# Performance work log

Measured on AMD Instinct MI355X. Metric: run time of the kernel, lower is better.

## Reference

```python
import jax, jax.numpy as jnp
import numpy as np

N_NODES = 50000
N_EDGES = 300000
D = 256          # in_dim = out_dim (residual)
DE = 256         # edge relation dim
K = 2            # num_kgs
H = 4            # heads
L = 2            # layers
DH = D // H


def _routed_linear(x, W, b, idx):
    # x:[E,din], W:[K,din,dout], b:[K,dout], idx:[E] in [0,K)
    # Compute all K branches (K is tiny) then select per edge.
    outs = jnp.einsum('ed,kdo->keo', x, W) + b[:, None, :]
    return outs[idx, jnp.arange(idx.shape[0])]


def _layernorm(x, g, b):
    mu = jnp.mean(x, axis=-1, keepdims=True)
    var = jnp.mean(jnp.square(x - mu), axis=-1, keepdims=True)
    return (x - mu) * jax.lax.rsqrt(var + 1e-5) * g + b


def _mga_layer(h, src, dst, kg_src, kg_dst, beta, rel,
               ln_g, ln_b, Wt, bt, Wq, bq, Wk, bk):
    N = h.shape[0]
    E = src.shape[0]
    residual = h
    hn = _layernorm(h, ln_g, ln_b)
    x_j = hn[src]                       # [E,D] gathered source feats
    x_i = hn[dst]                       # [E,D] gathered target feats
    # per-edge KG-routed transfer of concatenated (x_j, relation emb)
    xj_t = jax.nn.gelu(_routed_linear(jnp.concatenate([x_j, rel], axis=1), Wt, bt, kg_src),
                       approximate=False)
    q = _routed_linear(x_i, Wq, bq, kg_dst).reshape(E, H, DH)
    k = _routed_linear(xj_t, Wk, bk, kg_src).reshape(E, H, DH)
    # per-edge multi-head dot product, scaled by edge_beta_r then 1/sqrt(dh)
    att = jnp.sum(q * k, axis=-1) * beta[:, None] / jnp.sqrt(jnp.asarray(DH, h.dtype))  # [E,H]
    # scatter-softmax over incoming edges of each target node
    m = jax.ops.segment_max(att, dst, num_segments=N)          # [N,H]
    e = jnp.exp(att - m[dst])
    denom = jax.ops.segment_sum(e, dst, num_segments=N)        # [N,H]
    a = e / (denom[dst] + 1e-16)                                # [E,H]
    msg = (a[:, :, None] * xj_t.reshape(E, H, DH)).reshape(E, D)
    aggr = jax.ops.segment_sum(msg, dst, num_segments=N)        # [N,D]
    return residual + jax.nn.gelu(aggr, approximate=False)


def setup_inputs() -> dict:
    key = jax.random.key(0)
    ks = jax.random.split(key, 10)
    x = jax.random.normal(ks[0], (N_NODES, D), dtype=jnp.float32)
    edge_index = jax.random.randint(ks[1], (2, N_EDGES), 0, N_NODES, dtype=jnp.int32)
    edge_kg_index = jax.random.randint(ks[2], (2, N_EDGES), 0, K, dtype=jnp.int32)
    edge_beta_r = jax.random.uniform(ks[3], (N_EDGES,), dtype=jnp.float32)
    edge_rel_emb = jax.random.normal(ks[4], (N_EDGES, DE), dtype=jnp.float32)
    return {
        'x': x,
        'edge_index': edge_index,
        'edge_kg_index': edge_kg_index,
        'edge_beta_r': edge_beta_r,
        'edge_rel_emb': edge_rel_emb,
        'ln_g': jnp.ones((L, D), jnp.float32),
        'ln_b': jnp.zeros((L, D), jnp.float32),
        'Wt': jax.random.normal(ks[5], (L, K, D + DE, D), jnp.float32) / np.sqrt(D + DE),
        'bt': jnp.zeros((L, K, D), jnp.float32),
        'Wq': jax.random.normal(ks[6], (L, K, D, D), jnp.float32) / np.sqrt(D),
        'bq': jnp.zeros((L, K, D), jnp.float32),
        'Wk': jax.random.normal(ks[7], (L, K, D, D), jnp.float32) / np.sqrt(D),
        'bk': jnp.zeros((L, K, D), jnp.float32),
    }


def reference(x, edge_index, edge_kg_index, edge_beta_r, edge_rel_emb,
              ln_g, ln_b, Wt, bt, Wq, bq, Wk, bk):
    src, dst = edge_index[0], edge_index[1]          # j (source), i (target)
    kg_src, kg_dst = edge_kg_index[0], edge_kg_index[1]
    h = x  # dropout is identity in eval mode
    for l in range(L):
        h = _mga_layer(h, src, dst, kg_src, kg_dst, edge_beta_r, edge_rel_emb,
                       ln_g[l], ln_b[l], Wt[l], bt[l], Wq[l], bq[l], Wk[l], bk[l])
    return h
```

## Files before the change

kernel.cpp:

```cpp
#include <hip/hip_runtime.h>
#include <hip/hip_bf16.h>

#define NN 50000
#define NE 300000
#define DD 256
#define NCHUNK 293

typedef __hip_bfloat16 bf16;
typedef __attribute__((ext_vector_type(8))) short bf16x8;
typedef __attribute__((ext_vector_type(4))) float f32x4;

__device__ __forceinline__ float bf2f(bf16 v) { return __bfloat162float(v); }
__device__ __forceinline__ unsigned short f2b(float v) {
    bf16 t = __float2bfloat16(v);
    return *reinterpret_cast<unsigned short*>(&t);
}
__device__ __forceinline__ float b2f_bits(unsigned short u) {
    return __uint_as_float(((unsigned)u) << 16);
}
__device__ __forceinline__ float gelu_f(float v) {
    float v2 = v * v;
    float z  = v * fmaf(v2, 0.044715f, 1.0f) * 0.7978845608f;
    float e  = __expf(2.0f * z);
    float th = 1.0f - 2.0f / (e + 1.0f);
    return 0.5f * v * (1.0f + th);
}
__device__ __forceinline__ void gl2lds16(const uint4* g, uint4* l) {
    __builtin_amdgcn_global_load_lds(
        (const __attribute__((address_space(1))) void*)g,
        (__attribute__((address_space(3))) void*)l, 16, 0, 0);
}

__global__ void part_count(const int* __restrict__ kg, int* __restrict__ bcnt) {
    int base = blockIdx.x * 1024;
    __shared__ int wc[4];
    int t = threadIdx.x, wave = t >> 6, lane = t & 63;
    int cnt = 0;
    #pragma unroll
    for (int s = 0; s < 4; ++s) {
        int j = base + s * 256 + t;
        int is0 = (j < NE && kg[j] == 0) ? 1 : 0;
        unsigned long long m = __ballot(is0);
        if (lane == 0) cnt += __popcll(m);
    }
    if (lane == 0) wc[wave] = cnt;
    __syncthreads();
    if (t == 0) bcnt[blockIdx.x] = wc[0] + wc[1] + wc[2] + wc[3];
}

__global__ __launch_bounds__(512) void part_scan(const int* __restrict__ bcnt,
                                                 int* __restrict__ bofs,
                                                 int* __restrict__ meta, int n) {
    __shared__ int tmp[512];
    int t = threadIdx.x;
    int v = (t < n) ? bcnt[t] : 0;
    tmp[t] = v;
    __syncthreads();
    #pragma unroll
    for (int off = 1; off < 512; off <<= 1) {
        int u = (t >= off) ? tmp[t - off] : 0;
        __syncthreads();
        tmp[t] += u;
        __syncthreads();
    }
    if (t < n) bofs[t] = tmp[t] - v;
    if (t == n - 1) meta[0] = tmp[t];
}

__global__ void part_scatter(const int* __restrict__ kg, const int* __restrict__ bofs,
                             const int* __restrict__ meta, int* __restrict__ perm) {
    int base = blockIdx.x * 1024;
    int c0 = meta[0];
    __shared__ int wz[4];
    int t = threadIdx.x, wave = t >> 6, lane = t & 63;
    int zrun = bofs[blockIdx.x];
    for (int s = 0; s < 4; ++s) {
        int j = base + s * 256 + t;
        int valid = j < NE;
        int is0 = (valid && kg[j] == 0) ? 1 : 0;
        unsigned long long m = __ballot(is0);
        int zb = __popcll(m & ((1ull << lane) - 1ull));
        if (lane == 0) wz[wave] = __popcll(m);
        __syncthreads();
        int wbefore = 0;
        for (int w = 0; w < wave; ++w) wbefore += wz[w];
        int zeros_before = zrun + wbefore + zb;
        if (valid) {
            int pos = is0 ? zeros_before : (c0 + (j - zeros_before));
            perm[pos] = j;
        }
        int stepz = wz[0] + wz[1] + wz[2] + wz[3];
        __syncthreads();
        zrun += stepz;
    }
}

__global__ void deg_hist(const int* __restrict__ dst, int* __restrict__ deg) {
    int i = blockIdx.x * blockDim.x + threadIdx.x;
    if (i < NE) atomicAdd(&deg[dst[i]], 1);
}

__global__ __launch_bounds__(1024) void scan_nodes(const int* __restrict__ deg,
                                                   int* __restrict__ ofs,
                                                   int* __restrict__ cur) {
    __shared__ int pex[1025];
    int t = threadIdx.x;
    const int C = (NN + 1023) / 1024;
    int base = t * C;
    int s = 0;
    for (int j = 0; j < C; ++j) { int idx = base + j; if (idx < NN) s += deg[idx]; }
    pex[t + 1] = s;
    __syncthreads();
    if (t == 0) {
        pex[0] = 0;
        for (int i = 1; i <= 1024; ++i) pex[i] += pex[i - 1];
    }
    __syncthreads();
    int run = pex[t];
    for (int j = 0; j < C; ++j) {
        int idx = base + j;
        if (idx < NN) { ofs[idx] = run; cur[idx] = run; run += deg[idx]; }
    }
    if (t == 1023) ofs[NN] = pex[1024];
}

__global__ void csr_fill(const int* __restrict__ dst, int* __restrict__ cur,
                         int* __restrict__ eid) {
    int i = blockIdx.x * blockDim.x + threadIdx.x;
    if (i < NE) {
        int p = atomicAdd(&cur[dst[i]], 1);
        eid[p] = i;
    }
}

__global__ void f2b_vec_kernel(const float* __restrict__ in, ushort* __restrict__ out, long n4) {
    long i0 = (long)blockIdx.x * blockDim.x + threadIdx.x;
    long stride = (long)gridDim.x * blockDim.x;
    for (long i = i0; i < n4; i += stride) {
        float4 v = ((const float4*)in)[i];
        ushort4 o;
        o.x = f2b(v.x); o.y = f2b(v.y); o.z = f2b(v.z); o.w = f2b(v.w);
        ((ushort4*)out)[i] = o;
    }
}

__global__ void transpose_w_kernel(const float* __restrict__ in, ushort* __restrict__ out,
                                   int shift, long total) {
    long i0 = (long)blockIdx.x * blockDim.x + threadIdx.x;
    long stride = (long)gridDim.x * blockDim.x;
    long dmask = ((long)1 << shift) - 1;
    for (long i = i0; i < total; i += stride) {
        long d = i & dmask;
        long rest = i >> shift;
        long o = rest & 255;
        long s = rest >> 8;
        out[i] = f2b(in[((s << shift) + d) * 256 + o]);
    }
}

__global__ void fill_kernel(float* __restrict__ p, float v, int n) {
    for (int i = blockIdx.x * blockDim.x + threadIdx.x; i < n; i += gridDim.x * blockDim.x)
        p[i] = v;
}

__global__ __launch_bounds__(256) void lnx_kernel(const float* __restrict__ x,
        const float* __restrict__ g, const float* __restrict__ b,
        float* __restrict__ h, bf16* __restrict__ hn) {
    int n = blockIdx.x * 4 + (threadIdx.x >> 6);
    if (n >= NN) return;
    int t = threadIdx.x & 63;
    float4 v = ((const float4*)(x + (size_t)n * DD))[t];
    ((float4*)(h + (size_t)n * DD))[t] = v;
    float s  = v.x + v.y + v.z + v.w;
    float s2 = v.x * v.x + v.y * v.y + v.z * v.z + v.w * v.w;
    #pragma unroll
    for (int off = 32; off; off >>= 1) {
        s  += __shfl_down(s, off);
        s2 += __shfl_down(s2, off);
    }
    s = __shfl(s, 0); s2 = __shfl(s2, 0);
    float mu  = s * (1.f / DD);
    float var = s2 * (1.f / DD) - mu * mu;
    float rs  = rsqrtf(var + 1e-5f);
    float vv[4] = {v.x, v.y, v.z, v.w};
    ushort4 pk;
    unsigned short* pku = (unsigned short*)&pk;
    #pragma unroll
    for (int j = 0; j < 4; ++j) {
        int c = t * 4 + j;
        pku[j] = f2b((vv[j] - mu) * rs * g[c] + b[c]);
    }
    ((ushort4*)(hn + (size_t)n * DD))[t] = pk;
}

__global__ __launch_bounds__(512) void nodeq_mfma(
        const bf16* __restrict__ hn,
        const ushort* __restrict__ WqT, const float* __restrict__ bq,
        const ushort* __restrict__ WtT, const float* __restrict__ bt,
        ushort* __restrict__ qn, ushort* __restrict__ hw) {
    __shared__ uint4 xh[64 * 32];
    __shared__ float bqs[2][256], bts[2][256];
    int t = threadIdx.x;
    int n0 = blockIdx.x * 64;
    int wave = t >> 6, lane = t & 63;
    if (t < 256) { bqs[0][t] = bq[t]; bqs[1][t] = bq[256 + t]; }
    else { int c = t & 255; bts[0][c] = bt[c]; bts[1][c] = bt[256 + c]; }
    const uint4* hn4 = (const uint4*)hn;
    #pragma unroll
    for (int j = 0; j < 4; ++j) {
        int pr = wave * 4 + j;
        int r2 = pr * 2 + (lane >> 5);
        int node = n0 + r2; if (node >= NN) node = NN - 1;
        int s = lane & 31;
        gl2lds16(hn4 + (size_t)node * 32 + (s ^ (r2 & 7)), &xh[pr * 64]);
    }
    __syncthreads();
    int lr = lane & 15, lg = lane >> 4;
    const char* xhb = (const char*)xh;
    f32x4 acc[2][2][4];
    #pragma unroll
    for (int b = 0; b < 2; ++b)
        #pragma unroll
        for (int m = 0; m < 2; ++m)
            #pragma unroll
            for (int n = 0; n < 4; ++n) acc[b][m][n] = (f32x4){0.f, 0.f, 0.f, 0.f};
    {
        const ushort* tr0 = WtT + (size_t)(wave * 32 + lr) * 512 + lg * 8;
        const ushort* tr1 = WtT + (size_t)(wave * 32 + 16 + lr) * 512 + lg * 8;
        #pragma unroll
        for (int kk = 0; kk < 8; ++kk) {
            bf16x8 a00 = *(const bf16x8*)(tr0 + kk * 32);
            bf16x8 a01 = *(const bf16x8*)(tr1 + kk * 32);
            bf16x8 a10 = *(const bf16x8*)(tr0 + 131072 + kk * 32);
            bf16x8 a11 = *(const bf16x8*)(tr1 + 131072 + kk * 32);
            bf16x8 bfr[4];
            #pragma unroll
            for (int n = 0; n < 4; ++n) {
                int r = n * 16 + lr;
                bfr[n] = *(const bf16x8*)(xhb + r * 512 + (((kk * 4 + lg) ^ (r & 7)) << 4));
            }
            #pragma unroll
            for (int n = 0; n < 4; ++n) {
                acc[0][0][n] = __builtin_amdgcn_mfma_f32_16x16x32_bf16(a00, bfr[n], acc[0][0][n], 0, 0, 0);
                acc[0][1][n] = __builtin_amdgcn_mfma_f32_16x16x32_bf16(a01, bfr[n], acc[0][1][n], 0, 0, 0);
                acc[1][0][n] = __builtin_amdgcn_mfma_f32_16x16x32_bf16(a10, bfr[n], acc[1][0][n], 0, 0, 0);
                acc[1][1][n] = __builtin_amdgcn_mfma_f32_16x16x32_bf16(a11, bfr[n], acc[1][1][n], 0, 0, 0);
            }
        }
    }
    #pragma unroll
    for (int n = 0; n < 4; ++n) {
        int e = n * 16 + lr;
        int node = n0 + e;
        if (node < NN) {
            #pragma unroll
            for (int br = 0; br < 2; ++br)
                #pragma unroll
                for (int m = 0; m < 2; ++m) {
                    int ob = wave * 32 + m * 16 + lg * 4;
                    f32x4 a = acc[br][m][n];
                    ushort4 pk;
                    unsigned short* pu = (unsigned short*)&pk;
                    #pragma unroll
                    for (int r = 0; r < 4; ++r) pu[r] = f2b(a[r] + bts[br][ob + r]);
                    *(ushort4*)(hw + ((size_t)br * NN + node) * 256 + ob) = pk;
                }
        }
    }
    #pragma unroll
    for (int b = 0; b < 2; ++b)
        #pragma unroll
        for (int m = 0; m < 2; ++m)
            #pragma unroll
            for (int n = 0; n < 4; ++n) acc[b][m][n] = (f32x4){0.f, 0.f, 0.f, 0.f};
    {
        const ushort* qr0 = WqT + (size_t)(wave * 32 + lr) * 256 + lg * 8;
        const ushort* qr1 = WqT + (size_t)(wave * 32 + 16 + lr) * 256 + lg * 8;
        #pragma unroll
        for (int kk = 0; kk < 8; ++kk) {
            bf16x8 a00 = *(const bf16x8*)(qr0 + kk * 32);
            bf16x8 a01 = *(const bf16x8*)(qr1 + kk * 32);
            bf16x8 a10 = *(const bf16x8*)(qr0 + 65536 + kk * 32);
            bf16x8 a11 = *(const bf16x8*)(qr1 + 65536 + kk * 32);
            bf16x8 bfr[4];
            #pragma unroll
            for (int n = 0; n < 4; ++n) {
                int r = n * 16 + lr;
                bfr[n] = *(const bf16x8*)(xhb + r * 512 + (((kk * 4 + lg) ^ (r & 7)) << 4));
            }
            #pragma unroll
            for (int n = 0; n < 4; ++n) {
                acc[0][0][n] = __builtin_amdgcn_mfma_f32_16x16x32_bf16(a00, bfr[n], acc[0][0][n], 0, 0, 0);
                acc[0][1][n] = __builtin_amdgcn_mfma_f32_16x16x32_bf16(a01, bfr[n], acc[0][1][n], 0, 0, 0);
                acc[1][0][n] = __builtin_amdgcn_mfma_f32_16x16x32_bf16(a10, bfr[n], acc[1][0][n], 0, 0, 0);
                acc[1][1][n] = __builtin_amdgcn_mfma_f32_16x16x32_bf16(a11, bfr[n], acc[1][1][n], 0, 0, 0);
            }
        }
    }
    #pragma unroll
    for (int n = 0; n < 4; ++n) {
        int e = n * 16 + lr;
        int node = n0 + e;
        if (node < NN) {
            #pragma unroll
            for (int br = 0; br < 2; ++br)
                #pragma unroll
                for (int m = 0; m < 2; ++m) {
                    int ob = wave * 32 + m * 16 + lg * 4;
                    f32x4 a = acc[br][m][n];
                    ushort4 pk;
                    unsigned short* pu = (unsigned short*)&pk;
                    #pragma unroll
                    for (int r = 0; r < 4; ++r) pu[r] = f2b(a[r] + bqs[br][ob + r]);
                    *(ushort4*)(qn + ((size_t)br * NN + node) * 256 + ob) = pk;
                }
        }
    }
}

template<int RELB>
__global__ __launch_bounds__(512, 4) void transfer_mfma(
        const float* __restrict__ rel, const ushort* __restrict__ relb,
        const int* __restrict__ src, const int* __restrict__ dst,
        const int* __restrict__ kgd,
        const int* __restrict__ perm, const int* __restrict__ meta,
        const ushort* __restrict__ WtT,
        const ushort* __restrict__ WkT, const float* __restrict__ bk,
        const ushort* __restrict__ qn, const ushort* __restrict__ hw,
        const float* __restrict__ beta,
        bf16* __restrict__ xjt, float* __restrict__ att) {
    __shared__ uint4 xr[64 * 32];
    __shared__ float bks[256];
    __shared__ float patt[8][64];
    __shared__ int sge[64], ssrc[64], sdst[64], sgd[64], sval[64];
    int t = threadIdx.x;
    int c0 = meta[0];
    int tiles0 = (c0 + 63) >> 6;
    int tiles1 = (NE - c0 + 63) >> 6;
    int bid = blockIdx.x;
    if (bid >= tiles0 + tiles1) return;
    int kgt, start, end;
    if (bid < tiles0) { kgt = 0; start = bid * 64; end = c0; }
    else              { kgt = 1; start = c0 + (bid - tiles0) * 64; end = NE; }
    int wave = t >> 6, lane = t & 63;
    if (t < 64) {
        int pos = start + t;
        int v = pos < end;
        int ge = perm[v ? pos : end - 1];
        sge[t] = ge; sval[t] = v; ssrc[t] = src[ge]; sdst[t] = dst[ge]; sgd[t] = kgd[ge];
    } else if (t >= 256) {
        bks[t - 256] = bk[kgt * 256 + (t - 256)];
    }
    __syncthreads();
    if (RELB) {
        const uint4* rb4 = (const uint4*)relb;
        #pragma unroll
        for (int j = 0; j < 4; ++j) {
            int pr = wave * 4 + j;
            int r2 = pr * 2 + (lane >> 5);
            int s = lane & 31;
            gl2lds16(rb4 + (size_t)sge[r2] * 32 + (s ^ (r2 & 7)), &xr[pr * 64]);
        }
    } else {
        #pragma unroll
        for (int i = 0; i < 8; ++i) {
            int r = i * 8 + wave;
            float4 f = ((const float4*)(rel + (size_t)sge[r] * 256))[lane];
            ushort4 o;
            o.x = f2b(f.x); o.y = f2b(f.y); o.z = f2b(f.z); o.w = f2b(f.w);
            int s = lane >> 1;
            char* bp = (char*)&xr[r * 32] + (((s ^ (r & 7)) << 4) | ((lane & 1) << 3));
            *(ushort4*)bp = o;
        }
    }
    int lr = lane & 15, lg = lane >> 4;
    f32x4 acc[2][4];
    #pragma unroll
    for (int n = 0; n < 4; ++n) {
        int e = n * 16 + lr;
        size_t hb = ((size_t)kgt * NN + ssrc[e]) * 256;
        #pragma unroll
        for (int m = 0; m < 2; ++m) {
            int ob = wave * 32 + m * 16 + lg * 4;
            ushort4 w4 = *(const ushort4*)(hw + hb + ob);
            acc[m][n] = (f32x4){b2f_bits(w4.x), b2f_bits(w4.y), b2f_bits(w4.z), b2f_bits(w4.w)};
        }
    }
    ushort4 kv[2][4];
    #pragma unroll
    for (int n = 0; n < 4; ++n) {
        int e = n * 16 + lr;
        size_t qb = ((size_t)sgd[e] * NN + sdst[e]) * 256;
        #pragma unroll
        for (int m = 0; m < 2; ++m) {
            int ob = wave * 32 + m * 16 + lg * 4;
            kv[m][n] = *(const ushort4*)(qn + qb + ob);
        }
    }
    __syncthreads();
    const char* xrb = (const char*)xr;
    const ushort* wb = WtT + (size_t)kgt * 131072;
    const ushort* wrow0 = wb + (size_t)(wave * 32 + lr) * 512 + 256 + lg * 8;
    const ushort* wrow1 = wb + (size_t)(wave * 32 + 16 + lr) * 512 + 256 + lg * 8;
    __builtin_amdgcn_s_setprio(1);
    #pragma unroll
    for (int kk = 0; kk < 8; ++kk) {
        bf16x8 a0 = *(const bf16x8*)(wrow0 + kk * 32);
        bf16x8 a1 = *(const bf16x8*)(wrow1 + kk * 32);
        bf16x8 bfr[4];
        #pragma unroll
        for (int n = 0; n < 4; ++n) {
            int r = n * 16 + lr;
            bfr[n] = *(const bf16x8*)(xrb + r * 512 + (((kk * 4 + lg) ^ (r & 7)) << 4));
        }
        #pragma unroll
        for (int m = 0; m < 2; ++m)
            #pragma unroll
            for (int n = 0; n < 4; ++n)
                acc[m][n] = __builtin_amdgcn_mfma_f32_16x16x32_bf16((m ? a1 : a0), bfr[n], acc[m][n], 0, 0, 0);
    }
    __builtin_amdgcn_s_setprio(0);
    __syncthreads();
    char* xob = (char*)xr;
    #pragma unroll
    for (int n = 0; n < 4; ++n) {
        int e = n * 16 + lr;
        #pragma unroll
        for (int m = 0; m < 2; ++m) {
            int ob = wave * 32 + m * 16 + lg * 4;
            f32x4 a = acc[m][n];
            ushort4 pk;
            unsigned short* pu = (unsigned short*)&pk;
            #pragma unroll
            for (int r = 0; r < 4; ++r)
                pu[r] = f2b(gelu_f(a[r]));
            int bofs = ob * 2;
            int slot = ((bofs >> 4) ^ (e & 7));
            *(ushort4*)(xob + e * 512 + slot * 16 + (bofs & 15)) = pk;
        }
    }
    __syncthreads();
    uint4* xjv = (uint4*)xjt;
    #pragma unroll
    for (int i = 0; i < 4; ++i) {
        int flat = i * 512 + t;
        int r = flat >> 5, c = flat & 31;
        if (sval[r])
            xjv[(size_t)sge[r] * 32 + c] = *(const uint4*)(xob + r * 512 + ((c ^ (r & 7)) << 4));
    }
    #pragma unroll
    for (int m = 0; m < 2; ++m)
        #pragma unroll
        for (int n = 0; n < 4; ++n) acc[m][n] = (f32x4){0.f, 0.f, 0.f, 0.f};
    const ushort* kbw = WkT + (size_t)kgt * 65536;
    const ushort* kr0 = kbw + (size_t)(wave * 32 + lr) * 256 + lg * 8;
    const ushort* kr1 = kbw + (size_t)(wave * 32 + 16 + lr) * 256 + lg * 8;
    __builtin_amdgcn_s_setprio(1);
    #pragma unroll
    for (int kk = 0; kk < 8; ++kk) {
        bf16x8 a0 = *(const bf16x8*)(kr0 + kk * 32);
        bf16x8 a1 = *(const bf16x8*)(kr1 + kk * 32);
        bf16x8 bfr[4];
        #pragma unroll
        for (int n = 0; n < 4; ++n) {
            int r = n * 16 + lr;
            bfr[n] = *(const bf16x8*)(xob + r * 512 + (((kk * 4 + lg) ^ (r & 7)) << 4));
        }
        #pragma unroll
        for (int n = 0; n < 4; ++n) {
            acc[0][n] = __builtin_amdgcn_mfma_f32_16x16x32_bf16(a0, bfr[n], acc[0][n], 0, 0, 0);
            acc[1][n] = __builtin_amdgcn_mfma_f32_16x16x32_bf16(a1, bfr[n], acc[1][n], 0, 0, 0);
        }
    }
    __builtin_amdgcn_s_setprio(0);
    float p[4];
    #pragma unroll
    for (int n = 0; n < 4; ++n) {
        float s = 0.f;
        #pragma unroll
        for (int m = 0; m < 2; ++m) {
            int ob = wave * 32 + m * 16 + lg * 4;
            ushort4 qv = kv[m][n];
            f32x4 kcv = acc[m][n];
            s = fmaf(b2f_bits(qv.x), kcv[0] + bks[ob + 0], s);
            s = fmaf(b2f_bits(qv.y), kcv[1] + bks[ob + 1], s);
            s = fmaf(b2f_bits(qv.z), kcv[2] + bks[ob + 2], s);
            s = fmaf(b2f_bits(qv.w), kcv[3] + bks[ob + 3], s);
        }
        p[n] = s;
    }
    #pragma unroll
    for (int n = 0; n < 4; ++n) {
        p[n] += __shfl_xor(p[n], 16);
        p[n] += __shfl_xor(p[n], 32);
    }
    if (lane < 16) {
        #pragma unroll
        for (int n = 0; n < 4; ++n) patt[wave][n * 16 + lr] = p[n];
    }
    __syncthreads();
    if (t < 256) {
        int e = t & 63, h = t >> 6;
        if (sval[e]) {
            int ge = sge[e];
            att[(size_t)ge * 4 + h] = (patt[2 * h][e] + patt[2 * h + 1][e]) * beta[ge] * 0.125f;
        }
    }
}

template<int WRITE_HN>
__global__ __launch_bounds__(256) void aggregate_kernel(
        const float* __restrict__ att, const bf16* __restrict__ xjt,
        const int* __restrict__ eid, const int* __restrict__ ofs,
        float* __restrict__ h, const float* __restrict__ g, const float* __restrict__ b,
        bf16* __restrict__ hn) {
    int node = blockIdx.x * 4 + (threadIdx.x >> 6);
    if (node >= NN) return;
    int lane = threadIdx.x & 63;
    int hh = lane >> 4;
    int beg = ofs[node], end = ofs[node + 1];
    float m = -1e30f, den = 0.f;
    float a0 = 0.f, a1 = 0.f, a2 = 0.f, a3 = 0.f;
    for (int i = beg; i < end; ++i) {
        int e = eid[i];
        float av = att[(size_t)e * 4 + hh];
        if (av > m) {
            float r = __expf(m - av);
            den *= r; a0 *= r; a1 *= r; a2 *= r; a3 *= r;
            m = av;
        }
        float wgt = __expf(av - m);
        den += wgt;
        ushort4 v = *(const ushort4*)((const ushort*)xjt + (size_t)e * 256 + lane * 4);
        a0 = fmaf(wgt, b2f_bits(v.x), a0);
        a1 = fmaf(wgt, b2f_bits(v.y), a1);
        a2 = fmaf(wgt, b2f_bits(v.z), a2);
        a3 = fmaf(wgt, b2f_bits(v.w), a3);
    }
    float inv = 1.f / (den + 1e-16f);
    float4 hv = ((float4*)(h + (size_t)node * 256))[lane];
    hv.x += gelu_f(a0 * inv);
    hv.y += gelu_f(a1 * inv);
    hv.z += gelu_f(a2 * inv);
    hv.w += gelu_f(a3 * inv);
    ((float4*)(h + (size_t)node * 256))[lane] = hv;
    if (WRITE_HN) {
        float s  = hv.x + hv.y + hv.z + hv.w;
        float s2 = hv.x * hv.x + hv.y * hv.y + hv.z * hv.z + hv.w * hv.w;
        #pragma unroll
        for (int off = 32; off; off >>= 1) {
            s  += __shfl_down(s, off);
            s2 += __shfl_down(s2, off);
        }
        s = __shfl(s, 0); s2 = __shfl(s2, 0);
        float mu  = s * (1.f / DD);
        float var = s2 * (1.f / DD) - mu * mu;
        float rs  = rsqrtf(var + 1e-5f);
        float vv[4] = {hv.x, hv.y, hv.z, hv.w};
        ushort4 pk;
        unsigned short* pku = (unsigned short*)&pk;
        #pragma unroll
        for (int j = 0; j < 4; ++j) {
            int c = lane * 4 + j;
            pku[j] = f2b((vv[j] - mu) * rs * g[c] + b[c]);
        }
        ((ushort4*)(hn + (size_t)node * DD))[lane] = pk;
    }
}

extern "C" void kernel_launch(void* const* d_in, const int* in_sizes, int n_in,
                              void* d_out, int out_size, void* d_ws, size_t ws_size,
                              hipStream_t stream) {
    const float* x    = (const float*)d_in[0];
    const int*   ei   = (const int*)d_in[1];
    const int*   ekg  = (const int*)d_in[2];
    const float* beta = (const float*)d_in[3];
    const float* rel  = (const float*)d_in[4];
    const float* ln_g = (const float*)d_in[5];
    const float* ln_b = (const float*)d_in[6];
    const float* Wt   = (const float*)d_in[7];
    const float* bt   = (const float*)d_in[8];
    const float* Wq   = (const float*)d_in[9];
    const float* bq   = (const float*)d_in[10];
    const float* Wk   = (const float*)d_in[11];
    const float* bk   = (const float*)d_in[12];

    float* h = (float*)d_out;

    const int* srcp = ei;
    const int* dstp = ei + NE;
    const int* kgs  = ekg;
    const int* kgd  = ekg + NE;

    char* w = (char*)d_ws;
    float*  att   = (float*)w;  w += (size_t)NE * 4 * 4;
    bf16*   hn    = (bf16*)w;   w += (size_t)NN * DD * 2;
    bf16*   xjt   = (bf16*)w;   w += (size_t)NE * DD * 2;
    ushort* qn    = (ushort*)w; w += (size_t)2 * NN * DD * 2;
    ushort* hw    = (ushort*)w; w += (size_t)2 * NN * DD * 2;
    ushort* WtT   = (ushort*)w; w += (size_t)4 * 256 * 512 * 2;
    ushort* WqT   = (ushort*)w; w += (size_t)4 * 256 * 256 * 2;
    ushort* WkT   = (ushort*)w; w += (size_t)4 * 256 * 256 * 2;
    int* perm_src = (int*)w;    w += (size_t)NE * 4;
    int* bcnt0    = (int*)w;    w += NCHUNK * 4;
    int* bofs0    = (int*)w;    w += NCHUNK * 4;
    int* meta0    = (int*)w;    w += 64;
    int* deg      = (int*)w;    w += (size_t)NN * 4;
    int* ofs      = (int*)w;    w += (size_t)(NN + 1) * 4;
    int* cur      = (int*)w;    w += (size_t)NN * 4;
    int* eid      = (int*)w;    w += (size_t)NE * 4;
    size_t used = (size_t)(w - (char*)d_ws);
    ushort* relb = (ushort*)w;
    int use_relb = (ws_size >= used + (size_t)NE * DD * 2) ? 1 : 0;

    part_count<<<NCHUNK, 256, 0, stream>>>(kgs, bcnt0);
    part_scan<<<1, 512, 0, stream>>>(bcnt0, bofs0, meta0, NCHUNK);
    part_scatter<<<NCHUNK, 256, 0, stream>>>(kgs, bofs0, meta0, perm_src);

    fill_kernel<<<64, 256, 0, stream>>>((float*)deg, 0.f, NN);
    deg_hist<<<(NE + 255) / 256, 256, 0, stream>>>(dstp, deg);
    scan_nodes<<<1, 1024, 0, stream>>>(deg, ofs, cur);
    csr_fill<<<(NE + 255) / 256, 256, 0, stream>>>(dstp, cur, eid);

    if (use_relb)
        f2b_vec_kernel<<<2048, 256, 0, stream>>>(rel, relb, (long)NE * DD / 4);
    transpose_w_kernel<<<512, 256, 0, stream>>>(Wt, WtT, 9, (long)4 * 256 * 512);
    transpose_w_kernel<<<256, 256, 0, stream>>>(Wq, WqT, 8, (long)4 * 256 * 256);
    transpose_w_kernel<<<256, 256, 0, stream>>>(Wk, WkT, 8, (long)4 * 256 * 256);

    const int EBP = (NE + 126) / 64;
    const int QB  = (NN + 63) / 64;
    const int AGB = (NN + 3) / 4;

    lnx_kernel<<<AGB, 256, 0, stream>>>(x, ln_g, ln_b, h, hn);
    for (int l = 0; l < 2; ++l) {
        nodeq_mfma<<<QB, 512, 0, stream>>>(hn,
                WqT + (size_t)l * 2 * 256 * 256, bq + l * 512,
                WtT + (size_t)l * 2 * 256 * 512, bt + l * 512, qn, hw);
        if (use_relb)
            transfer_mfma<1><<<EBP, 512, 0, stream>>>(rel, relb, srcp, dstp, kgd,
                    perm_src, meta0,
                    WtT + (size_t)l * 2 * 256 * 512,
                    WkT + (size_t)l * 2 * 256 * 256, bk + l * 512, qn, hw, beta, xjt, att);
        else
            transfer_mfma<0><<<EBP, 512, 0, stream>>>(rel, relb, srcp, dstp, kgd,
                    perm_src, meta0,
                    WtT + (size_t)l * 2 * 256 * 512,
                    WkT + (size_t)l * 2 * 256 * 256, bk + l * 512, qn, hw, beta, xjt, att);
        if (l == 0)
            aggregate_kernel<1><<<AGB, 256, 0, stream>>>(att, xjt, eid, ofs, h,
                    ln_g + DD, ln_b + DD, hn);
        else
            aggregate_kernel<0><<<AGB, 256, 0, stream>>>(att, xjt, eid, ofs, h,
                    ln_g, ln_b, hn);
    }
}
```

Measured before the change: 1.172 ms.

## Sort edges by (kg, src) via counting sort instead of kg-only partition

Replaces the stable kg-only partition of edges with a counting sort keyed on (kg_src, src node). It builds a 2*NN histogram with atomics, scans it, and scatters edge ids. Within each KG group, edges that share a source node end up adjacent, so the transfer kernel's gathers of rel/hw rows for the same source should get better cache locality. In exchange it adds atomic histogram and scatter passes, a larger single-block scan, and a non-deterministic order within each bucket. The node-degree scan is also switched to the shared generic scan kernel.

```diff
diff --git a/kernel.cpp b/kernel.cpp
--- a/kernel.cpp
+++ b/kernel.cpp
@@ -4,7 +4,6 @@
 #define NN 50000
 #define NE 300000
 #define DD 256
-#define NCHUNK 293
 
 typedef __hip_bfloat16 bf16;
 typedef __attribute__((ext_vector_type(8))) short bf16x8;
@@ -31,97 +30,54 @@
         (__attribute__((address_space(3))) void*)l, 16, 0, 0);
 }
 
-__global__ void part_count(const int* __restrict__ kg, int* __restrict__ bcnt) {
-    int base = blockIdx.x * 1024;
-    __shared__ int wc[4];
-    int t = threadIdx.x, wave = t >> 6, lane = t & 63;
-    int cnt = 0;
-    #pragma unroll
-    for (int s = 0; s < 4; ++s) {
-        int j = base + s * 256 + t;
-        int is0 = (j < NE && kg[j] == 0) ? 1 : 0;
-        unsigned long long m = __ballot(is0);
-        if (lane == 0) cnt += __popcll(m);
-    }
-    if (lane == 0) wc[wave] = cnt;
+__global__ void hist2_kernel(const int* __restrict__ kg, const int* __restrict__ src,
+                             int* __restrict__ hist) {
+    int i = blockIdx.x * blockDim.x + threadIdx.x;
+    if (i < NE) atomicAdd(&hist[kg[i] * NN + src[i]], 1);
+}
+
+__global__ __launch_bounds__(1024) void scan_big(const int* __restrict__ in,
+                                                 int* __restrict__ ofs,
+                                                 int* __restrict__ cur, int n) {
+    __shared__ int part[1024];
+    int t = threadIdx.x;
+    int C = (n + 1023) >> 10;
+    int base = t * C;
+    int s = 0;
+    for (int j = 0; j < C; ++j) { int idx = base + j; if (idx < n) s += in[idx]; }
+    part[t] = s;
     __syncthreads();
-    if (t == 0) bcnt[blockIdx.x] = wc[0] + wc[1] + wc[2] + wc[3];
-}
-
-__global__ __launch_bounds__(512) void part_scan(const int* __restrict__ bcnt,
-                                                 int* __restrict__ bofs,
-                                                 int* __restrict__ meta, int n) {
-    __shared__ int tmp[512];
-    int t = threadIdx.x;
-    int v = (t < n) ? bcnt[t] : 0;
-    tmp[t] = v;
-    __syncthreads();
-    #pragma unroll
-    for (int off = 1; off < 512; off <<= 1) {
-        int u = (t >= off) ? tmp[t - off] : 0;
+    #pragma unroll
+    for (int off = 1; off < 1024; off <<= 1) {
+        int u = (t >= off) ? part[t - off] : 0;
         __syncthreads();
-        tmp[t] += u;
+        part[t] += u;
         __syncthreads();
     }
-    if (t < n) bofs[t] = tmp[t] - v;
-    if (t == n - 1) meta[0] = tmp[t];
-}
-
-__global__ void part_scatter(const int* __restrict__ kg, const int* __restrict__ bofs,
-                             const int* __restrict__ meta, int* __restrict__ perm) {
-    int base = blockIdx.x * 1024;
-    int c0 = meta[0];
-    __shared__ int wz[4];
-    int t = threadIdx.x, wave = t >> 6, lane = t & 63;
-    int zrun = bofs[blockIdx.x];
-    for (int s = 0; s < 4; ++s) {
-        int j = base + s * 256 + t;
-        int valid = j < NE;
-        int is0 = (valid && kg[j] == 0) ? 1 : 0;
-        unsigned long long m = __ballot(is0);
-        int zb = __popcll(m & ((1ull << lane) - 1ull));
-        if (lane == 0) wz[wave] = __popcll(m);
-        __syncthreads();
-        int wbefore = 0;
-        for (int w = 0; w < wave; ++w) wbefore += wz[w];
-        int zeros_before = zrun + wbefore + zb;
-        if (valid) {
-            int pos = is0 ? zeros_before : (c0 + (j - zeros_before));
-            perm[pos] = j;
-        }
-        int stepz = wz[0] + wz[1] + wz[2] + wz[3];
-        __syncthreads();
-        zrun += stepz;
+    int run = (t == 0) ? 0 : part[t - 1];
+    for (int j = 0; j < C; ++j) {
+        int idx = base + j;
+        if (idx < n) {
+            ofs[idx] = run;
+            if (cur) cur[idx] = run;
+            run += in[idx];
+        }
+    }
+    if (t == 1023) ofs[n] = part[1023];
+}
+
+__global__ void scatter2_kernel(const int* __restrict__ kg, const int* __restrict__ src,
+                                int* __restrict__ cur, int* __restrict__ perm) {
+    int i = blockIdx.x * blockDim.x + threadIdx.x;
+    if (i < NE) {
+        int p = atomicAdd(&cur[kg[i] * NN + src[i]], 1);
+        perm[p] = i;
     }
 }
 
 __global__ void deg_hist(const int* __restrict__ dst, int* __restrict__ deg) {
     int i = blockIdx.x * blockDim.x + threadIdx.x;
     if (i < NE) atomicAdd(&deg[dst[i]], 1);
-}
-
-__global__ __launch_bounds__(1024) void scan_nodes(const int* __restrict__ deg,
-                                                   int* __restrict__ ofs,
-                                                   int* __restrict__ cur) {
-    __shared__ int pex[1025];
-    int t = threadIdx.x;
-    const int C = (NN + 1023) / 1024;
-    int base = t * C;
-    int s = 0;
-    for (int j = 0; j < C; ++j) { int idx = base + j; if (idx < NN) s += deg[idx]; }
-    pex[t + 1] = s;
-    __syncthreads();
-    if (t == 0) {
-        pex[0] = 0;
-        for (int i = 1; i <= 1024; ++i) pex[i] += pex[i - 1];
-    }
-    __syncthreads();
-    int run = pex[t];
-    for (int j = 0; j < C; ++j) {
-        int idx = base + j;
-        if (idx < NN) { ofs[idx] = run; cur[idx] = run; run += deg[idx]; }
-    }
-    if (t == 1023) ofs[NN] = pex[1024];
 }
 
 __global__ void csr_fill(const int* __restrict__ dst, int* __restrict__ cur,
@@ -602,9 +558,9 @@
     ushort* WqT   = (ushort*)w; w += (size_t)4 * 256 * 256 * 2;
     ushort* WkT   = (ushort*)w; w += (size_t)4 * 256 * 256 * 2;
     int* perm_src = (int*)w;    w += (size_t)NE * 4;
-    int* bcnt0    = (int*)w;    w += NCHUNK * 4;
-    int* bofs0    = (int*)w;    w += NCHUNK * 4;
-    int* meta0    = (int*)w;    w += 64;
+    int* hist2    = (int*)w;    w += (size_t)2 * NN * 4;
+    int* ofs2     = (int*)w;    w += (size_t)(2 * NN + 1) * 4;
+    int* cur2     = (int*)w;    w += (size_t)2 * NN * 4;
     int* deg      = (int*)w;    w += (size_t)NN * 4;
     int* ofs      = (int*)w;    w += (size_t)(NN + 1) * 4;
     int* cur      = (int*)w;    w += (size_t)NN * 4;
@@ -613,13 +569,14 @@
     ushort* relb = (ushort*)w;
     int use_relb = (ws_size >= used + (size_t)NE * DD * 2) ? 1 : 0;
 
-    part_count<<<NCHUNK, 256, 0, stream>>>(kgs, bcnt0);
-    part_scan<<<1, 512, 0, stream>>>(bcnt0, bofs0, meta0, NCHUNK);
-    part_scatter<<<NCHUNK, 256, 0, stream>>>(kgs, bofs0, meta0, perm_src);
+    fill_kernel<<<128, 256, 0, stream>>>((float*)hist2, 0.f, 2 * NN);
+    hist2_kernel<<<(NE + 255) / 256, 256, 0, stream>>>(kgs, srcp, hist2);
+    scan_big<<<1, 1024, 0, stream>>>(hist2, ofs2, cur2, 2 * NN);
+    scatter2_kernel<<<(NE + 255) / 256, 256, 0, stream>>>(kgs, srcp, cur2, perm_src);
 
     fill_kernel<<<64, 256, 0, stream>>>((float*)deg, 0.f, NN);
     deg_hist<<<(NE + 255) / 256, 256, 0, stream>>>(dstp, deg);
-    scan_nodes<<<1, 1024, 0, stream>>>(deg, ofs, cur);
+    scan_big<<<1, 1024, 0, stream>>>(deg, ofs, cur, NN);
     csr_fill<<<(NE + 255) / 256, 256, 0, stream>>>(dstp, cur, eid);
 
     if (use_relb)
@@ -639,12 +596,12 @@
                 WtT + (size_t)l * 2 * 256 * 512, bt + l * 512, qn, hw);
         if (use_relb)
             transfer_mfma<1><<<EBP, 512, 0, stream>>>(rel, relb, srcp, dstp, kgd,
-                    perm_src, meta0,
+                    perm_src, ofs2 + NN,
                     WtT + (size_t)l * 2 * 256 * 512,
                     WkT + (size_t)l * 2 * 256 * 256, bk + l * 512, qn, hw, beta, xjt, att);
         else
             transfer_mfma<0><<<EBP, 512, 0, stream>>>(rel, relb, srcp, dstp, kgd,
-                    perm_src, meta0,
+                    perm_src, ofs2 + NN,
                     WtT + (size_t)l * 2 * 256 * 512,
                     WkT + (size_t)l * 2 * 256 * 256, bk + l * 512, qn, hw, beta, xjt, att);
         if (l == 0)
```

After: 1.431 ms. 1.22x slower.
